# Kernel optimization log

Measured on AMD Instinct MI355X. Metric: run time of the kernel, lower is better.

Reference implementation:

```python
import jax, jax.numpy as jnp
import numpy as np
from jax import lax

STEPLIM = 10
TOL = 1e-4
EPS = 1e-12


def setup_inputs() -> dict:
    key = jax.random.key(0)
    k1, k2 = jax.random.split(key)
    psrc = jax.random.normal(k1, (8, 2048, 3), dtype=jnp.float32)
    ptgt = jax.random.normal(k2, (8, 2048, 3), dtype=jnp.float32)
    return {"psrc": psrc, "ptgt": ptgt}


def _kabsch(p, q):
    # Rigid transform (R, t) minimizing ||q - (R p + t)|| via SVD (Kabsch).
    # p, q: [B, N, 3] matched point pairs.
    cs = jnp.mean(p, axis=-2, keepdims=True)  # [B,1,3]
    ct = jnp.mean(q, axis=-2, keepdims=True)
    H = jnp.einsum('bni,bnj->bij', p - cs, q - ct)  # [B,3,3]
    U, S, Vt = jnp.linalg.svd(H, full_matrices=False)
    V = jnp.swapaxes(Vt, -1, -2)
    Ut = jnp.swapaxes(U, -1, -2)
    d = jnp.sign(jnp.linalg.det(V @ Ut))  # [B], reflection fix
    scale = jnp.stack([jnp.ones_like(d), jnp.ones_like(d), d], axis=-1)  # [B,3]
    R = (V * scale[:, None, :]) @ Ut  # V @ diag(1,1,d) @ U^T
    t = ct[:, 0, :] - jnp.einsum('bij,bj->bi', R, cs[:, 0, :])
    return R, t


def _nn(pc, ptgt):
    # Brute-force 1-NN of each pc point in ptgt. Returns (dist [B,Ns], idx [B,Ns]).
    # GEMM-form squared distances: ||a||^2 + ||b||^2 - 2 a.b
    a2 = jnp.sum(pc * pc, axis=-1)  # [B,Ns]
    b2 = jnp.sum(ptgt * ptgt, axis=-1)  # [B,Nt]
    d2 = a2[:, :, None] + b2[:, None, :] - 2.0 * jnp.einsum('bnd,bmd->bnm', pc, ptgt)
    d2 = jnp.maximum(d2, EPS)
    idx = jnp.argmin(d2, axis=-1)  # [B,Ns]
    dist = jnp.sqrt(jnp.min(d2, axis=-1))
    return dist, idx


def reference(psrc, ptgt):
    B = psrc.shape[0]

    def step(carry, _):
        pc, err, done = carry
        dist, idx = _nn(pc, ptgt)
        errnew = jnp.mean(dist, axis=-1)  # [B]
        done_new = jnp.logical_or(done, jnp.all(jnp.abs(errnew - err) < TOL))
        matched = jnp.take_along_axis(ptgt, idx[:, :, None], axis=1)  # [B,Ns,3]
        R, t = _kabsch(pc, matched)
        pc_upd = jnp.einsum('bij,bnj->bni', R, pc) + t[:, None, :]
        pc_new = jnp.where(done_new, pc, pc_upd)
        err_new = jnp.where(done_new, err, errnew)
        return (pc_new, err_new, done_new), None

    init = (psrc, jnp.zeros((B,), psrc.dtype), jnp.array(False))
    (pc_final, _, _), _ = lax.scan(step, init, None, length=STEPLIM)

    # Final transform from original psrc to converged point cloud.
    R, t = _kabsch(psrc, pc_final)
    return jnp.concatenate([R, t[:, :, None]], axis=-1)  # [B,3,4]
```

## Files before the change

kernel.cpp:

```cpp
#include <hip/hip_runtime.h>
#include <math.h>

#define NB 8
#define NP 2048
#define GRID 256
#define TOLF 1e-4f
#define EPSF 1e-12f

#define AL(p)   __hip_atomic_load((p), __ATOMIC_RELAXED, __HIP_MEMORY_SCOPE_AGENT)
#define AS(p,v) __hip_atomic_store((p), (v), __ATOMIC_RELAXED, __HIP_MEMORY_SCOPE_AGENT)

__device__ inline float3 xform_pt(const float* __restrict__ T,
                                  float x, float y, float z) {
    float3 r;
    r.x = fmaf(T[0], x, fmaf(T[1], y, fmaf(T[2], z, T[9])));
    r.y = fmaf(T[3], x, fmaf(T[4], y, fmaf(T[5], z, T[10])));
    r.z = fmaf(T[6], x, fmaf(T[7], y, fmaf(T[8], z, T[11])));
    return r;
}

__device__ void kabsch3x3(const double Spq[9], const double Sp[3], const double Sq[3],
                          double R[9], double t[3]) {
    const double invN = 1.0 / (double)NP;
    double cs[3], ct[3];
#pragma unroll
    for (int i = 0; i < 3; ++i) { cs[i] = Sp[i] * invN; ct[i] = Sq[i] * invN; }
    double H[9];
#pragma unroll
    for (int i = 0; i < 3; ++i)
#pragma unroll
        for (int j = 0; j < 3; ++j)
            H[i * 3 + j] = Spq[i * 3 + j] - (double)NP * cs[i] * ct[j];

    double Bc[3][3], V[3][3];
#pragma unroll
    for (int j = 0; j < 3; ++j)
#pragma unroll
        for (int i = 0; i < 3; ++i) {
            Bc[j][i] = H[i * 3 + j];
            V[j][i]  = (i == j) ? 1.0 : 0.0;
        }
    for (int sweep = 0; sweep < 16; ++sweep) {
        bool rotated = false;
        for (int p = 0; p < 2; ++p)
            for (int q = p + 1; q < 3; ++q) {
                double app = 0, aqq = 0, apq = 0;
#pragma unroll
                for (int i = 0; i < 3; ++i) {
                    app += Bc[p][i] * Bc[p][i];
                    aqq += Bc[q][i] * Bc[q][i];
                    apq += Bc[p][i] * Bc[q][i];
                }
                if (apq * apq > 1e-60 + 1e-28 * app * aqq) {
                    rotated = true;
                    double tau = (aqq - app) / (2.0 * apq);
                    double tt  = (tau >= 0 ? 1.0 : -1.0) / (fabs(tau) + sqrt(1.0 + tau * tau));
                    double c   = 1.0 / sqrt(1.0 + tt * tt);
                    double sn  = c * tt;
#pragma unroll
                    for (int i = 0; i < 3; ++i) {
                        double bp = Bc[p][i], bq = Bc[q][i];
                        Bc[p][i] = c * bp - sn * bq;
                        Bc[q][i] = sn * bp + c * bq;
                        double vp = V[p][i], vq = V[q][i];
                        V[p][i] = c * vp - sn * vq;
                        V[q][i] = sn * vp + c * vq;
                    }
                }
            }
        if (!rotated) break;
    }
    double sv[3], U[3][3];
#pragma unroll
    for (int j = 0; j < 3; ++j) {
        sv[j] = sqrt(Bc[j][0] * Bc[j][0] + Bc[j][1] * Bc[j][1] + Bc[j][2] * Bc[j][2]);
        double inv = sv[j] > 0.0 ? 1.0 / sv[j] : 0.0;
#pragma unroll
        for (int i = 0; i < 3; ++i) U[j][i] = Bc[j][i] * inv;
    }
    double detH = H[0] * (H[4] * H[8] - H[5] * H[7])
                - H[1] * (H[3] * H[8] - H[5] * H[6])
                + H[2] * (H[3] * H[7] - H[4] * H[6]);
    double d = (detH >= 0.0) ? 1.0 : -1.0;
    int o[3] = {0, 1, 2};
    if (sv[o[0]] < sv[o[1]]) { int tmp = o[0]; o[0] = o[1]; o[1] = tmp; }
    if (sv[o[0]] < sv[o[2]]) { int tmp = o[0]; o[0] = o[2]; o[2] = tmp; }
    if (sv[o[1]] < sv[o[2]]) { int tmp = o[1]; o[1] = o[2]; o[2] = tmp; }
    double sg[3] = {1.0, 1.0, d};
#pragma unroll
    for (int i = 0; i < 3; ++i)
#pragma unroll
        for (int j = 0; j < 3; ++j) {
            double acc = 0.0;
#pragma unroll
            for (int k = 0; k < 3; ++k) acc += sg[k] * V[o[k]][i] * U[o[k]][j];
            R[i * 3 + j] = acc;
        }
#pragma unroll
    for (int i = 0; i < 3; ++i)
        t[i] = ct[i] - (R[i * 3 + 0] * cs[0] + R[i * 3 + 1] * cs[1] + R[i * 3 + 2] * cs[2]);
}

__global__ __launch_bounds__(256) void icp_init(unsigned* __restrict__ flags) {
    flags[threadIdx.x] = 0u;
}

__global__ __launch_bounds__(256, 2) void icp_main(
        const float* __restrict__ psrc, const float* __restrict__ ptgt,
        double* __restrict__ partial,
        unsigned* __restrict__ flags,
        double* __restrict__ Tcs,
        unsigned* __restrict__ cbits) {
    __shared__ float4 tg[2080];
    __shared__ float4 ps[64];
    __shared__ float2 comb[32][66];
    __shared__ float  TcL[12];
    __shared__ double TcA[12];

    const int tid   = threadIdx.x;
    const int blk   = blockIdx.x;
    const int b     = blk >> 5;
    const int sc    = blk & 31;
    const int slice = tid & 31;
    const int g     = tid >> 5;

    float errL = 0.0f;

    const float* tb = ptgt + b * NP * 3;
    for (int j = tid; j < NP; j += 256) {
        float tx = tb[3 * j + 0], ty = tb[3 * j + 1], tz = tb[3 * j + 2];
        tg[j + (j >> 6)] = make_float4(tx, ty, tz,
                                       0.5f * (tx * tx + ty * ty + tz * tz));
    }
    if (tid < 12) {
        float idv = (tid == 0 || tid == 4 || tid == 8) ? 1.0f : 0.0f;
        TcL[tid] = idv;
        TcA[tid] = (double)idv;
        if (sc == 0) AS(&Tcs[(b * 11 + 0) * 12 + tid], (double)idv);
    }
    __syncthreads();

    for (int it = 1; it <= 10; ++it) {
        if (tid < 64) {
            const float* pp = psrc + (b * NP + sc * 64 + tid) * 3;
            float3 P = xform_pt(TcL, pp[0], pp[1], pp[2]);
            ps[tid] = make_float4(P.x, P.y, P.z,
                                  P.x * P.x + P.y * P.y + P.z * P.z);
        }
        __syncthreads();

        float sx[8], sy[8], sz[8], sm[8];
        int jm[8];
#pragma unroll
        for (int k = 0; k < 8; ++k) {
            float4 P = ps[g * 8 + k];
            sx[k] = P.x; sy[k] = P.y; sz[k] = P.z;
            sm[k] = INFINITY; jm[k] = 0;
        }
        const int base = slice * 65, jbase = slice * 64;
#pragma unroll 4
        for (int i = 0; i < 64; ++i) {
            float4 t = tg[base + i];
            int j = jbase + i;
#pragma unroll
            for (int k = 0; k < 8; ++k) {
                float s = fmaf(-sx[k], t.x, fmaf(-sy[k], t.y, fmaf(-sz[k], t.z, t.w)));
                if (s < sm[k]) { sm[k] = s; jm[k] = j; }
            }
        }
#pragma unroll
        for (int k = 0; k < 8; ++k)
            comb[slice][g * 8 + k] = make_float2(sm[k], __int_as_float(jm[k]));
        __syncthreads();

        double* pbase = partial + (size_t)(it & 1) * GRID * 16;

        if (tid < 64) {
            float fb = INFINITY; int fj = 0;
#pragma unroll 8
            for (int q = 0; q < 32; ++q) {
                float2 e = comb[q][tid];
                if (e.x < fb) { fb = e.x; fj = __float_as_int(e.y); }
            }
            float4 P = ps[tid];
            float d2 = fmaf(2.0f, fb, P.w);
            float dist = sqrtf(fmaxf(d2, EPSF));
            float4 Q = tg[fj + (fj >> 6)];

            double v[16];
            v[0] = dist;
            v[1] = P.x; v[2] = P.y; v[3] = P.z;
            v[4] = Q.x; v[5] = Q.y; v[6] = Q.z;
            v[7]  = (double)P.x * Q.x; v[8]  = (double)P.x * Q.y; v[9]  = (double)P.x * Q.z;
            v[10] = (double)P.y * Q.x; v[11] = (double)P.y * Q.y; v[12] = (double)P.y * Q.z;
            v[13] = (double)P.z * Q.x; v[14] = (double)P.z * Q.y; v[15] = (double)P.z * Q.z;
#pragma unroll
            for (int k = 0; k < 16; ++k) {
                double x = v[k];
#pragma unroll
                for (int off = 32; off > 0; off >>= 1) x += __shfl_down(x, off);
                v[k] = x;
            }
            if (tid == 0) {
                double* dst = pbase + blk * 16;
#pragma unroll
                for (int k = 0; k < 16; ++k) AS(dst + k, v[k]);
                asm volatile("s_waitcnt vmcnt(0)" ::: "memory");
                AS(&flags[blk], (unsigned)it);
            }
            bool ok;
            do {
                ok = (tid < 32) ? (AL(&flags[b * 32 + tid]) >= (unsigned)it) : true;
                if (!__all(ok)) __builtin_amdgcn_s_sleep(1); else break;
            } while (true);

            if (tid < 32) {
                double acc[16];
                const double* pp2 = pbase + (b * 32 + tid) * 16;
#pragma unroll
                for (int k = 0; k < 16; ++k) acc[k] = AL(pp2 + k);
#pragma unroll
                for (int k = 0; k < 16; ++k) {
                    double x = acc[k];
                    x += __shfl_down(x, 16);
                    x += __shfl_down(x, 8);
                    x += __shfl_down(x, 4);
                    x += __shfl_down(x, 2);
                    x += __shfl_down(x, 1);
                    acc[k] = x;
                }
                if (tid == 0) {
                    float errnew = (float)(acc[0] * (1.0 / (double)NP));
                    unsigned cb = (fabsf(errnew - errL) < TOLF) ? 1u : 0u;
                    errL = errnew;
                    double R[9], t[3];
                    kabsch3x3(&acc[7], &acc[1], &acc[4], R, t);
                    double To[12];
#pragma unroll
                    for (int k = 0; k < 12; ++k) To[k] = TcA[k];
#pragma unroll
                    for (int i = 0; i < 3; ++i) {
#pragma unroll
                        for (int j = 0; j < 3; ++j)
                            TcA[i * 3 + j] = R[i * 3 + 0] * To[0 + j]
                                           + R[i * 3 + 1] * To[3 + j]
                                           + R[i * 3 + 2] * To[6 + j];
                        TcA[9 + i] = R[i * 3 + 0] * To[9] + R[i * 3 + 1] * To[10]
                                   + R[i * 3 + 2] * To[11] + t[i];
                    }
                    if (sc == 0) {
#pragma unroll
                        for (int k = 0; k < 12; ++k)
                            AS(&Tcs[(b * 11 + it) * 12 + k], TcA[k]);
                        AS(&cbits[b * 16 + it], cb);
                    }
                }
            }
        }
        __syncthreads();
        if (tid < 12) TcL[tid] = (float)TcA[tid];
        __syncthreads();
    }
}

__global__ __launch_bounds__(64) void icp_resolve(const double* __restrict__ Tcs,
                                                  const unsigned* __restrict__ cbits,
                                                  float* __restrict__ out) {
    __shared__ int ksel;
    int tid = threadIdx.x;
    if (tid == 0) {
        int sel = 10;
        for (int t = 1; t <= 10; ++t) {
            bool all = true;
            for (int b2 = 0; b2 < NB; ++b2) all = all && (cbits[b2 * 16 + t] != 0u);
            if (all) { sel = t - 1; break; }
        }
        ksel = sel;
    }
    __syncthreads();
    if (tid < NB) {
        const double* T = Tcs + ((size_t)tid * 11 + ksel) * 12;
        float* o = out + tid * 12;
#pragma unroll
        for (int i = 0; i < 3; ++i) {
#pragma unroll
            for (int j = 0; j < 3; ++j) o[i * 4 + j] = (float)T[i * 3 + j];
            o[i * 4 + 3] = (float)T[9 + i];
        }
    }
}

extern "C" void kernel_launch(void* const* d_in, const int* in_sizes, int n_in,
                              void* d_out, int out_size, void* d_ws, size_t ws_size,
                              hipStream_t stream) {
    const float* psrc = (const float*)d_in[0];
    const float* ptgt = (const float*)d_in[1];
    float* out = (float*)d_out;

    char* ws = (char*)d_ws;
    size_t off = 0;
    double* partial = (double*)(ws + off); off += 2ull * GRID * 16 * sizeof(double);
    unsigned* flags = (unsigned*)(ws + off); off += GRID * sizeof(unsigned);
    double* Tcs   = (double*)(ws + off);   off += (size_t)NB * 11 * 12 * sizeof(double);
    unsigned* cbits = (unsigned*)(ws + off); off += NB * 16 * sizeof(unsigned);

    icp_init<<<1, 256, 0, stream>>>(flags);
    icp_main<<<GRID, 256, 0, stream>>>(psrc, ptgt, partial, flags, Tcs, cbits);
    icp_resolve<<<1, 64, 0, stream>>>(Tcs, cbits, out);
}
```

Before: 187.8 us.

## Double threads per block, split target scan, run Jacobi SVD in fp32

Blocks grow from 256 to 512 threads, so each thread scans 32 targets instead of 64 and the cross-slice combine covers 64 partial results. The grid-barrier spin moves to a separate wavefront (threads 64-127), with a block sync before the reduction. The one-sided Jacobi SVD inside Kabsch now runs in fp32 with fewer sweeps, avoiding slow double-precision math on the serial single-thread path. The risks are lower SVD precision near degenerate cases, a longer combine loop, and one resident block per SIMD group limiting latency hiding.

```diff
diff --git a/kernel.cpp b/kernel.cpp
--- a/kernel.cpp
+++ b/kernel.cpp
@@ -4,6 +4,7 @@
 #define NB 8
 #define NP 2048
 #define GRID 256
+#define THREADS 512
 #define TOLF 1e-4f
 #define EPSF 1e-12f
 
@@ -25,44 +26,45 @@
     double cs[3], ct[3];
 #pragma unroll
     for (int i = 0; i < 3; ++i) { cs[i] = Sp[i] * invN; ct[i] = Sq[i] * invN; }
-    double H[9];
+    double Hd[9];
 #pragma unroll
     for (int i = 0; i < 3; ++i)
 #pragma unroll
         for (int j = 0; j < 3; ++j)
-            H[i * 3 + j] = Spq[i * 3 + j] - (double)NP * cs[i] * ct[j];
-
-    double Bc[3][3], V[3][3];
+            Hd[i * 3 + j] = Spq[i * 3 + j] - (double)NP * cs[i] * ct[j];
+
+    float Bc[3][3], V[3][3];
 #pragma unroll
     for (int j = 0; j < 3; ++j)
 #pragma unroll
         for (int i = 0; i < 3; ++i) {
-            Bc[j][i] = H[i * 3 + j];
-            V[j][i]  = (i == j) ? 1.0 : 0.0;
-        }
-    for (int sweep = 0; sweep < 16; ++sweep) {
+            Bc[j][i] = (float)Hd[i * 3 + j];
+            V[j][i]  = (i == j) ? 1.0f : 0.0f;
+        }
+    for (int sweep = 0; sweep < 12; ++sweep) {
         bool rotated = false;
         for (int p = 0; p < 2; ++p)
             for (int q = p + 1; q < 3; ++q) {
-                double app = 0, aqq = 0, apq = 0;
+                float app = 0.f, aqq = 0.f, apq = 0.f;
 #pragma unroll
                 for (int i = 0; i < 3; ++i) {
-                    app += Bc[p][i] * Bc[p][i];
-                    aqq += Bc[q][i] * Bc[q][i];
-                    apq += Bc[p][i] * Bc[q][i];
+                    app = fmaf(Bc[p][i], Bc[p][i], app);
+                    aqq = fmaf(Bc[q][i], Bc[q][i], aqq);
+                    apq = fmaf(Bc[p][i], Bc[q][i], apq);
                 }
-                if (apq * apq > 1e-60 + 1e-28 * app * aqq) {
+                if (apq * apq > 1e-24f + 1e-12f * app * aqq) {
                     rotated = true;
-                    double tau = (aqq - app) / (2.0 * apq);
-                    double tt  = (tau >= 0 ? 1.0 : -1.0) / (fabs(tau) + sqrt(1.0 + tau * tau));
-                    double c   = 1.0 / sqrt(1.0 + tt * tt);
-                    double sn  = c * tt;
+                    float tau = (aqq - app) / (2.0f * apq);
+                    float tt  = (tau >= 0.f ? 1.0f : -1.0f) /
+                                (fabsf(tau) + sqrtf(fmaf(tau, tau, 1.0f)));
+                    float c   = 1.0f / sqrtf(fmaf(tt, tt, 1.0f));
+                    float sn  = c * tt;
 #pragma unroll
                     for (int i = 0; i < 3; ++i) {
-                        double bp = Bc[p][i], bq = Bc[q][i];
+                        float bp = Bc[p][i], bq = Bc[q][i];
                         Bc[p][i] = c * bp - sn * bq;
                         Bc[q][i] = sn * bp + c * bq;
-                        double vp = V[p][i], vq = V[q][i];
+                        float vp = V[p][i], vq = V[q][i];
                         V[p][i] = c * vp - sn * vq;
                         V[q][i] = sn * vp + c * vq;
                     }
@@ -70,31 +72,31 @@
             }
         if (!rotated) break;
     }
-    double sv[3], U[3][3];
+    float sv[3], U[3][3];
 #pragma unroll
     for (int j = 0; j < 3; ++j) {
-        sv[j] = sqrt(Bc[j][0] * Bc[j][0] + Bc[j][1] * Bc[j][1] + Bc[j][2] * Bc[j][2]);
-        double inv = sv[j] > 0.0 ? 1.0 / sv[j] : 0.0;
+        sv[j] = sqrtf(Bc[j][0] * Bc[j][0] + Bc[j][1] * Bc[j][1] + Bc[j][2] * Bc[j][2]);
+        float inv = sv[j] > 0.f ? 1.0f / sv[j] : 0.f;
 #pragma unroll
         for (int i = 0; i < 3; ++i) U[j][i] = Bc[j][i] * inv;
     }
-    double detH = H[0] * (H[4] * H[8] - H[5] * H[7])
-                - H[1] * (H[3] * H[8] - H[5] * H[6])
-                + H[2] * (H[3] * H[7] - H[4] * H[6]);
-    double d = (detH >= 0.0) ? 1.0 : -1.0;
+    double detH = Hd[0] * (Hd[4] * Hd[8] - Hd[5] * Hd[7])
+                - Hd[1] * (Hd[3] * Hd[8] - Hd[5] * Hd[6])
+                + Hd[2] * (Hd[3] * Hd[7] - Hd[4] * Hd[6]);
+    float d = (detH >= 0.0) ? 1.0f : -1.0f;
     int o[3] = {0, 1, 2};
     if (sv[o[0]] < sv[o[1]]) { int tmp = o[0]; o[0] = o[1]; o[1] = tmp; }
     if (sv[o[0]] < sv[o[2]]) { int tmp = o[0]; o[0] = o[2]; o[2] = tmp; }
     if (sv[o[1]] < sv[o[2]]) { int tmp = o[1]; o[1] = o[2]; o[2] = tmp; }
-    double sg[3] = {1.0, 1.0, d};
+    float sg[3] = {1.0f, 1.0f, d};
 #pragma unroll
     for (int i = 0; i < 3; ++i)
 #pragma unroll
         for (int j = 0; j < 3; ++j) {
-            double acc = 0.0;
+            float acc = 0.0f;
 #pragma unroll
             for (int k = 0; k < 3; ++k) acc += sg[k] * V[o[k]][i] * U[o[k]][j];
-            R[i * 3 + j] = acc;
+            R[i * 3 + j] = (double)acc;
         }
 #pragma unroll
     for (int i = 0; i < 3; ++i)
@@ -105,15 +107,15 @@
     flags[threadIdx.x] = 0u;
 }
 
-__global__ __launch_bounds__(256, 2) void icp_main(
+__global__ __launch_bounds__(THREADS, 1) void icp_main(
         const float* __restrict__ psrc, const float* __restrict__ ptgt,
         double* __restrict__ partial,
         unsigned* __restrict__ flags,
         double* __restrict__ Tcs,
         unsigned* __restrict__ cbits) {
-    __shared__ float4 tg[2080];
+    __shared__ float4 tg[2112];
     __shared__ float4 ps[64];
-    __shared__ float2 comb[32][66];
+    __shared__ float2 comb[64][66];
     __shared__ float  TcL[12];
     __shared__ double TcA[12];
 
@@ -121,15 +123,15 @@
     const int blk   = blockIdx.x;
     const int b     = blk >> 5;
     const int sc    = blk & 31;
-    const int slice = tid & 31;
-    const int g     = tid >> 5;
+    const int slice = tid & 63;
+    const int g     = tid >> 6;
 
     float errL = 0.0f;
 
     const float* tb = ptgt + b * NP * 3;
-    for (int j = tid; j < NP; j += 256) {
+    for (int j = tid; j < NP; j += THREADS) {
         float tx = tb[3 * j + 0], ty = tb[3 * j + 1], tz = tb[3 * j + 2];
-        tg[j + (j >> 6)] = make_float4(tx, ty, tz,
+        tg[j + (j >> 5)] = make_float4(tx, ty, tz,
                                        0.5f * (tx * tx + ty * ty + tz * tz));
     }
     if (tid < 12) {
@@ -157,9 +159,9 @@
             sx[k] = P.x; sy[k] = P.y; sz[k] = P.z;
             sm[k] = INFINITY; jm[k] = 0;
         }
-        const int base = slice * 65, jbase = slice * 64;
+        const int base = slice * 33, jbase = slice * 32;
 #pragma unroll 4
-        for (int i = 0; i < 64; ++i) {
+        for (int i = 0; i < 32; ++i) {
             float4 t = tg[base + i];
             int j = jbase + i;
 #pragma unroll
@@ -178,14 +180,14 @@
         if (tid < 64) {
             float fb = INFINITY; int fj = 0;
 #pragma unroll 8
-            for (int q = 0; q < 32; ++q) {
+            for (int q = 0; q < 64; ++q) {
                 float2 e = comb[q][tid];
                 if (e.x < fb) { fb = e.x; fj = __float_as_int(e.y); }
             }
             float4 P = ps[tid];
             float d2 = fmaf(2.0f, fb, P.w);
             float dist = sqrtf(fmaxf(d2, EPSF));
-            float4 Q = tg[fj + (fj >> 6)];
+            float4 Q = tg[fj + (fj >> 5)];
 
             double v[16];
             v[0] = dist;
@@ -208,52 +210,55 @@
                 asm volatile("s_waitcnt vmcnt(0)" ::: "memory");
                 AS(&flags[blk], (unsigned)it);
             }
+        } else if (tid < 128) {
+            int l = tid - 64;
             bool ok;
             do {
-                ok = (tid < 32) ? (AL(&flags[b * 32 + tid]) >= (unsigned)it) : true;
+                ok = (l < 32) ? (AL(&flags[b * 32 + l]) >= (unsigned)it) : true;
                 if (!__all(ok)) __builtin_amdgcn_s_sleep(1); else break;
             } while (true);
-
-            if (tid < 32) {
-                double acc[16];
-                const double* pp2 = pbase + (b * 32 + tid) * 16;
-#pragma unroll
-                for (int k = 0; k < 16; ++k) acc[k] = AL(pp2 + k);
-#pragma unroll
-                for (int k = 0; k < 16; ++k) {
-                    double x = acc[k];
-                    x += __shfl_down(x, 16);
-                    x += __shfl_down(x, 8);
-                    x += __shfl_down(x, 4);
-                    x += __shfl_down(x, 2);
-                    x += __shfl_down(x, 1);
-                    acc[k] = x;
+        }
+        __syncthreads();
+
+        if (tid < 32) {
+            double acc[16];
+            const double* pp2 = pbase + (b * 32 + tid) * 16;
+#pragma unroll
+            for (int k = 0; k < 16; ++k) acc[k] = AL(pp2 + k);
+#pragma unroll
+            for (int k = 0; k < 16; ++k) {
+                double x = acc[k];
+                x += __shfl_down(x, 16);
+                x += __shfl_down(x, 8);
+                x += __shfl_down(x, 4);
+                x += __shfl_down(x, 2);
+                x += __shfl_down(x, 1);
+                acc[k] = x;
+            }
+            if (tid == 0) {
+                float errnew = (float)(acc[0] * (1.0 / (double)NP));
+                unsigned cb = (fabsf(errnew - errL) < TOLF) ? 1u : 0u;
+                errL = errnew;
+                double R[9], t[3];
+                kabsch3x3(&acc[7], &acc[1], &acc[4], R, t);
+                double To[12];
+#pragma unroll
+                for (int k = 0; k < 12; ++k) To[k] = TcA[k];
+#pragma unroll
+                for (int i = 0; i < 3; ++i) {
+#pragma unroll
+                    for (int j = 0; j < 3; ++j)
+                        TcA[i * 3 + j] = R[i * 3 + 0] * To[0 + j]
+                                       + R[i * 3 + 1] * To[3 + j]
+                                       + R[i * 3 + 2] * To[6 + j];
+                    TcA[9 + i] = R[i * 3 + 0] * To[9] + R[i * 3 + 1] * To[10]
+                               + R[i * 3 + 2] * To[11] + t[i];
                 }
-                if (tid == 0) {
-                    float errnew = (float)(acc[0] * (1.0 / (double)NP));
-                    unsigned cb = (fabsf(errnew - errL) < TOLF) ? 1u : 0u;
-                    errL = errnew;
-                    double R[9], t[3];
-                    kabsch3x3(&acc[7], &acc[1], &acc[4], R, t);
-                    double To[12];
-#pragma unroll
-                    for (int k = 0; k < 12; ++k) To[k] = TcA[k];
-#pragma unroll
-                    for (int i = 0; i < 3; ++i) {
-#pragma unroll
-                        for (int j = 0; j < 3; ++j)
-                            TcA[i * 3 + j] = R[i * 3 + 0] * To[0 + j]
-                                           + R[i * 3 + 1] * To[3 + j]
-                                           + R[i * 3 + 2] * To[6 + j];
-                        TcA[9 + i] = R[i * 3 + 0] * To[9] + R[i * 3 + 1] * To[10]
-                                   + R[i * 3 + 2] * To[11] + t[i];
-                    }
-                    if (sc == 0) {
-#pragma unroll
-                        for (int k = 0; k < 12; ++k)
-                            AS(&Tcs[(b * 11 + it) * 12 + k], TcA[k]);
-                        AS(&cbits[b * 16 + it], cb);
-                    }
+                if (sc == 0) {
+#pragma unroll
+                    for (int k = 0; k < 12; ++k)
+                        AS(&Tcs[(b * 11 + it) * 12 + k], TcA[k]);
+                    AS(&cbits[b * 16 + it], cb);
                 }
             }
         }
@@ -305,6 +310,6 @@
     unsigned* cbits = (unsigned*)(ws + off); off += NB * 16 * sizeof(unsigned);
 
     icp_init<<<1, 256, 0, stream>>>(flags);
-    icp_main<<<GRID, 256, 0, stream>>>(psrc, ptgt, partial, flags, Tcs, cbits);
+    icp_main<<<GRID, THREADS, 0, stream>>>(psrc, ptgt, partial, flags, Tcs, cbits);
     icp_resolve<<<1, 64, 0, stream>>>(Tcs, cbits, out);
 }
```

Measured after the change: 183.0 us. 2.6% less time.
